# Performance work log

Hardware: AMD Instinct MI355X
Metric: run time of the kernel (lower is better)

## Reference

```python
import math
import jax, jax.numpy as jnp
import numpy as np

HID, HEADS, HEAD_DIM, MLP = 768, 12, 64, 3072
ROT_AXIS = HEAD_DIM // 4  # 16 rotary dims per spatial axis, 48 total
MAX_FREQ = 256.0
EPS_GN, EPS_LN = 1e-6, 1e-5


def setup_inputs() -> dict:
    key = jax.random.key(0)
    ks = jax.random.split(key, 5)
    B, H, W, D = 2, 12, 12, 12
    s = 0.02
    return {
        "x": jax.random.normal(ks[0], (B, HID, H, W, D), jnp.float32),
        "norm1_w": jnp.ones((HID,), jnp.float32),
        "w_fused": jax.random.normal(ks[1], (MLP + 3 * HID, HID), jnp.float32) * s,
        "b_fused": jnp.zeros((MLP + 3 * HID,), jnp.float32),
        "q_gamma": jnp.ones((HEAD_DIM,), jnp.float32),
        "q_beta": jnp.zeros((HEAD_DIM,), jnp.float32),
        "k_gamma": jnp.ones((HEAD_DIM,), jnp.float32),
        "k_beta": jnp.zeros((HEAD_DIM,), jnp.float32),
        "w_attn": jax.random.normal(ks[2], (HID, HID), jnp.float32) * s,
        "w_ff": jax.random.normal(ks[3], (HID, MLP // 2), jnp.float32) * s,
        "b_ff": jnp.zeros((HID,), jnp.float32),
    }


def _layernorm(t, gamma, beta):
    mu = jnp.mean(t, axis=-1, keepdims=True)
    var = jnp.mean((t - mu) ** 2, axis=-1, keepdims=True)
    return (t - mu) / jnp.sqrt(var + EPS_LN) * gamma + beta


def _rotate_half(t):
    # interleaved pairs: (x1, x2) -> (-x2, x1)
    t2 = t.reshape(t.shape[:-1] + (t.shape[-1] // 2, 2))
    return jnp.stack((-t2[..., 1], t2[..., 0]), axis=-1).reshape(t.shape)


def _axial_freqs(H, W, D):
    base = jnp.linspace(1.0, MAX_FREQ / 2, ROT_AXIS // 2) * math.pi  # (8,)
    def ax(n):
        pos = jnp.linspace(-1.0, 1.0, n)
        f = pos[:, None] * base[None, :]          # (n, 8)
        return jnp.repeat(f, 2, axis=-1)          # (n, 16)
    fH = jnp.broadcast_to(ax(H)[:, None, None, :], (H, W, D, ROT_AXIS))
    fW = jnp.broadcast_to(ax(W)[None, :, None, :], (H, W, D, ROT_AXIS))
    fD = jnp.broadcast_to(ax(D)[None, None, :, :], (H, W, D, ROT_AXIS))
    return jnp.concatenate((fH, fW, fD), axis=-1)  # (H, W, D, 48)


def _apply_rope(t, cosf, sinf, rot_dim):
    t_mid, t_right = t[..., :rot_dim], t[..., rot_dim:]
    t_mid = t_mid * cosf + _rotate_half(t_mid) * sinf
    return jnp.concatenate((t_mid, t_right), axis=-1)


def reference(x, norm1_w, w_fused, b_fused, q_gamma, q_beta, k_gamma, k_beta,
              w_attn, w_ff, b_ff):
    B, C, H, W, D = x.shape
    residual = x
    # RMSGroupNorm: norm axes are the spatial dims only (per-channel RMS)
    rms = jnp.sqrt(jnp.mean(x ** 2, axis=(2, 3, 4), keepdims=True) + EPS_GN)
    xn = x / rms * norm1_w[None, :, None, None, None]
    xn = jnp.transpose(xn, (0, 2, 3, 4, 1))  # b h w d c
    fused = jnp.einsum('bhwdc,oc->bhwdo', xn, w_fused) + b_fused
    ff = fused[..., :MLP]
    q = fused[..., MLP:MLP + HID]
    k = fused[..., MLP + HID:MLP + 2 * HID]
    v = fused[..., MLP + 2 * HID:]
    def to_heads(t):  # b h w d (he c) -> b he h w d c
        return jnp.transpose(t.reshape(B, H, W, D, HEADS, HEAD_DIM), (0, 4, 1, 2, 3, 5))
    q, k, v = to_heads(q), to_heads(k), to_heads(v)
    q = _layernorm(q, q_gamma, q_beta)
    k = _layernorm(k, k_gamma, k_beta)
    freqs = _axial_freqs(H, W, D)                 # (H, W, D, 48)
    cosf, sinf = jnp.cos(freqs), jnp.sin(freqs)
    rot_dim = freqs.shape[-1]
    q = _apply_rope(q, cosf, sinf, rot_dim)
    k = _apply_rope(k, cosf, sinf, rot_dim)
    S = H * W * D
    q = q.reshape(B, HEADS, S, HEAD_DIM)
    k = k.reshape(B, HEADS, S, HEAD_DIM)
    v = v.reshape(B, HEADS, S, HEAD_DIM)
    scale = 1.0 / math.sqrt(HEAD_DIM)
    attn = jax.nn.softmax(jnp.einsum('bhsc,bhtc->bhst', q, k) * scale, axis=-1)
    att = jnp.einsum('bhst,bhtc->bhsc', attn, v)
    att = jnp.transpose(att, (0, 2, 1, 3)).reshape(B, H, W, D, HID)
    attn_out = jnp.einsum('bhwdc,oc->bhwdo', att, w_attn)
    ff_x, gate = jnp.split(ff, 2, axis=-1)
    ff_act = jax.nn.silu(gate) * ff_x
    ff_out = jnp.einsum('bhwdc,oc->bhwdo', ff_act, w_ff) + b_ff
    out = attn_out + ff_out
    out = jnp.transpose(out, (0, 4, 1, 2, 3)) + residual
    return out
```

## Files before the change

kernel.cpp:

```cpp
#include <hip/hip_runtime.h>

using bf16 = __bf16;
typedef __attribute__((ext_vector_type(8))) __bf16 bf16x8;
typedef __attribute__((ext_vector_type(4))) float f32x4;

#define HID    768
#define S_TOT  1728
#define MLP_   3072
#define NFUSED 5376
#define HEADS  12
#define HDIM   64
#define ROT    48
#define KCAT   2304

__device__ __forceinline__ void gload16(const void* g, void* l) {
  __builtin_amdgcn_global_load_lds((__attribute__((address_space(1))) void*)g,
                                   (__attribute__((address_space(3))) void*)l,
                                   16, 0, 0);
}

__device__ __forceinline__ float fexp2(float x) {
  float r; asm("v_exp_f32 %0, %1" : "=v"(r) : "v"(x)); return r;
}

__device__ __forceinline__ float wsum64(float v) {
  #pragma unroll
  for (int d = 32; d; d >>= 1) v += __shfl_xor(v, d);
  return v;
}

__global__ __launch_bounds__(256) void k_conv(const float* __restrict__ wf,
    const float* __restrict__ wa, const float* __restrict__ wff,
    bf16* __restrict__ owf, bf16* __restrict__ wcat) {
  int i = blockIdx.x * 256 + threadIdx.x;
  const int nf = NFUSED * HID, na = HID * HID, nff = HID * (MLP_ / 2);
  if (i < nf)  owf[i] = (bf16)wf[i];
  if (i < na)  wcat[(i / HID) * KCAT + (i % HID)] = (bf16)wa[i];
  if (i < nff) wcat[(i / (MLP_ / 2)) * KCAT + HID + (i % (MLP_ / 2))] = (bf16)wff[i];
}

__global__ __launch_bounds__(256) void k_rms(const float* __restrict__ x,
    const float* __restrict__ w, float* __restrict__ scale) {
  int bc = blockIdx.x;
  const float* xp = x + (size_t)bc * S_TOT;
  float s = 0.f;
  for (int i = threadIdx.x; i < S_TOT; i += 256) { float v = xp[i]; s += v * v; }
  s = wsum64(s);
  __shared__ float red[4];
  int lane = threadIdx.x & 63, wv = threadIdx.x >> 6;
  if (lane == 0) red[wv] = s;
  __syncthreads();
  if (threadIdx.x == 0) {
    float t = red[0] + red[1] + red[2] + red[3];
    scale[bc] = w[bc % HID] * rsqrtf(t * (1.f / S_TOT) + 1e-6f);
  }
}

__global__ __launch_bounds__(256) void k_xpose(const float* __restrict__ x,
    const float* __restrict__ scale, bf16* __restrict__ xn) {
  __shared__ float t[32][33];
  int b = blockIdx.z, st = blockIdx.x * 32, ct = blockIdx.y * 32;
  int tx = threadIdx.x & 31, ty = threadIdx.x >> 5;
  #pragma unroll
  for (int i = 0; i < 4; ++i) {
    int c = ct + ty + i * 8;
    t[ty + i * 8][tx] = x[((size_t)b * HID + c) * S_TOT + st + tx] * scale[b * HID + c];
  }
  __syncthreads();
  #pragma unroll
  for (int i = 0; i < 4; ++i) {
    int s = st + ty + i * 8;
    xn[((size_t)b * S_TOT + s) * HID + ct + tx] = (bf16)t[tx][ty + i * 8];
  }
}

__global__ __launch_bounds__(256) void k_rope(float* __restrict__ ct, float* __restrict__ st) {
  int i = blockIdx.x * 256 + threadIdx.x;
  if (i >= S_TOT * ROT) return;
  int s = i / ROT, j = i % ROT;
  int axis = j >> 4, pr = (j & 15) >> 1;
  float base = 3.14159265358979323846f * (1.f + pr * (127.f / 7.f));
  int coord = axis == 0 ? (s / 144) : axis == 1 ? ((s / 12) % 12) : (s % 12);
  float pos = -1.f + coord * (2.f / 11.f);
  float f = pos * base;
  ct[i] = cosf(f); st[i] = sinf(f);
}

template <int BN, int NMAJOR, int MINB>
__global__ __launch_bounds__(256, MINB) void k_gemm(const bf16* __restrict__ A,
    const bf16* __restrict__ Bw, const float* __restrict__ bias,
    void* __restrict__ OutV, int M, int N, int K) {
  extern __shared__ __align__(16) char smem[];
  bf16* aL = (bf16*)smem;
  bf16* bL = (bf16*)(smem + 2 * 8192);
  constexpr int NT = BN / 32;
  constexpr int LPS = 2 + BN / 64;
  const int nT = K / 32;
  int nwg = gridDim.x;
  int cq = nwg >> 3, crr = nwg & 7;
  int xcd = blockIdx.x & 7, pos = blockIdx.x >> 3;
  int idx = (xcd < crr ? xcd * (cq + 1) : crr * (cq + 1) + (xcd - crr) * cq) + pos;
  int ntn = N / BN, nmt = M / 128;
  int m0, n0;
  if (NMAJOR) { n0 = (idx / nmt) * BN; m0 = (idx % nmt) * 128; }
  else        { m0 = (idx / ntn) * 128; n0 = (idx % ntn) * BN; }
  int lane = threadIdx.x & 63, wv = threadIdx.x >> 6;
  int wm = (wv >> 1) * 64, wn = (wv & 1) * (BN / 2);
  int arow = lane >> 2;
  int acs = ((lane & 3) ^ ((lane >> 3) & 3)) * 8;
  int r16 = lane & 15, g8 = (lane >> 4) * 8;
  int swz = ((r16 >> 1) & 3) << 3;
  const bf16* Ag = A + (size_t)m0 * K;
  const bf16* Bg = Bw + (size_t)n0 * K;
  auto stage = [&](int p, int t) {
    int kk = t * 32;
    #pragma unroll
    for (int i = 0; i < 2; ++i) {
      int rb = wv * 32 + i * 16;
      gload16(Ag + (size_t)(rb + arow) * K + kk + acs, aL + p * 4096 + rb * 32);
    }
    #pragma unroll
    for (int i = 0; i < BN / 64; ++i) {
      int rb = wv * (BN / 4) + i * 16;
      gload16(Bg + (size_t)(rb + arow) * K + kk + acs, bL + p * (BN * 32) + rb * 32);
    }
  };
  f32x4 acc[4][NT] = {};
  int p = 0;
  stage(0, 0);
  for (int t = 0; t < nT; ++t) {
    if (t + 1 < nT) {
      stage(p ^ 1, t + 1);
      if constexpr (LPS == 5) asm volatile("s_waitcnt vmcnt(5)\ns_barrier" ::: "memory");
      else if constexpr (LPS == 4) asm volatile("s_waitcnt vmcnt(4)\ns_barrier" ::: "memory");
      else                     asm volatile("s_waitcnt vmcnt(3)\ns_barrier" ::: "memory");
    } else {
      asm volatile("s_waitcnt vmcnt(0)\ns_barrier" ::: "memory");
    }
    bf16x8 af[4], bfr[NT];
    #pragma unroll
    for (int mi = 0; mi < 4; ++mi)
      af[mi] = *(const bf16x8*)(aL + p * 4096 + (wm + mi * 16 + r16) * 32 + (g8 ^ swz));
    #pragma unroll
    for (int ni = 0; ni < NT; ++ni)
      bfr[ni] = *(const bf16x8*)(bL + p * (BN * 32) + (wn + ni * 16 + r16) * 32 + (g8 ^ swz));
    __builtin_amdgcn_s_setprio(1);
    #pragma unroll
    for (int mi = 0; mi < 4; ++mi)
      #pragma unroll
      for (int ni = 0; ni < NT; ++ni)
        acc[mi][ni] = __builtin_amdgcn_mfma_f32_16x16x32_bf16(af[mi], bfr[ni], acc[mi][ni], 0, 0, 0);
    __builtin_amdgcn_s_setprio(0);
    asm volatile("s_barrier" ::: "memory");
    p ^= 1;
  }
  int cr = (lane >> 4) * 4;
  #pragma unroll
  for (int mi = 0; mi < 4; ++mi)
    #pragma unroll
    for (int ni = 0; ni < NT; ++ni) {
      int col = n0 + wn + ni * 16 + r16;
      float bv = bias[col];
      #pragma unroll
      for (int j = 0; j < 4; ++j) {
        int row = m0 + wm + mi * 16 + cr + j;
        ((bf16*)OutV)[(size_t)row * N + col] = (bf16)(acc[mi][ni][j] + bv);
      }
    }
}

__global__ __launch_bounds__(256, 3) void k_gemmO(const bf16* __restrict__ A,
    const bf16* __restrict__ Bw, const float* __restrict__ bias,
    float* __restrict__ Out, const float* __restrict__ X, int M, int N, int K) {
  extern __shared__ __align__(16) char smem[];
  bf16* aL = (bf16*)smem;
  bf16* bL = (bf16*)(smem + 2 * 16384);
  const int nT = K / 64;
  int nwg = gridDim.x;
  int cq = nwg >> 3, crr = nwg & 7;
  int xcd = blockIdx.x & 7, pos = blockIdx.x >> 3;
  int idx = (xcd < crr ? xcd * (cq + 1) : crr * (cq + 1) + (xcd - crr) * cq) + pos;
  int ntn = N / 64;
  int m0 = (idx / ntn) * 128, n0 = (idx % ntn) * 64;
  int lane = threadIdx.x & 63, wv = threadIdx.x >> 6;
  int wm = (wv >> 1) * 64, wn = (wv & 1) * 32;
  int rg = lane >> 3, ch = lane & 7;
  int scs = (ch ^ rg) * 8;
  int r16 = lane & 15, g8 = (lane >> 4) * 8;
  const bf16* Ag = A + (size_t)m0 * K;
  const bf16* Bg = Bw + (size_t)n0 * K;
  auto stage = [&](int p, int t) {
    int kk = t * 64;
    #pragma unroll
    for (int i = 0; i < 4; ++i) {
      int rb = wv * 32 + i * 8;
      gload16(Ag + (size_t)(rb + rg) * K + kk + scs, aL + p * 8192 + rb * 64);
    }
    #pragma unroll
    for (int i = 0; i < 2; ++i) {
      int rb = wv * 16 + i * 8;
      gload16(Bg + (size_t)(rb + rg) * K + kk + scs, bL + p * 4096 + rb * 64);
    }
  };
  f32x4 acc[4][2] = {};
  int p = 0;
  stage(0, 0);
  for (int t = 0; t < nT; ++t) {
    if (t + 1 < nT) {
      stage(p ^ 1, t + 1);
      asm volatile("s_waitcnt vmcnt(6)\ns_barrier" ::: "memory");
    } else {
      asm volatile("s_waitcnt vmcnt(0)\ns_barrier" ::: "memory");
    }
    bf16x8 af[4][2], bfr[2][2];
    #pragma unroll
    for (int kc = 0; kc < 2; ++kc) {
      int ce = ((kc * 4 + (lane >> 4)) ^ (r16 & 7)) * 8;
      #pragma unroll
      for (int mi = 0; mi < 4; ++mi)
        af[mi][kc] = *(const bf16x8*)(aL + p * 8192 + (wm + mi * 16 + r16) * 64 + ce);
      #pragma unroll
      for (int ni = 0; ni < 2; ++ni)
        bfr[ni][kc] = *(const bf16x8*)(bL + p * 4096 + (wn + ni * 16 + r16) * 64 + ce);
    }
    __builtin_amdgcn_s_setprio(1);
    #pragma unroll
    for (int kc = 0; kc < 2; ++kc)
      #pragma unroll
      for (int mi = 0; mi < 4; ++mi)
        #pragma unroll
        for (int ni = 0; ni < 2; ++ni)
          acc[mi][ni] = __builtin_amdgcn_mfma_f32_16x16x32_bf16(af[mi][kc], bfr[ni][kc], acc[mi][ni], 0, 0, 0);
    __builtin_amdgcn_s_setprio(0);
    asm volatile("s_barrier" ::: "memory");
    p ^= 1;
  }
  int cr = (lane >> 4) * 4;
  float* tb = (float*)smem;
  __syncthreads();
  #pragma unroll
  for (int mi = 0; mi < 4; ++mi)
    #pragma unroll
    for (int ni = 0; ni < 2; ++ni) {
      int c = wn + ni * 16 + r16;
      float bv = bias[n0 + c];
      #pragma unroll
      for (int j = 0; j < 4; ++j)
        tb[c * 129 + wm + mi * 16 + cr + j] = acc[mi][ni][j] + bv;
    }
  __syncthreads();
  for (int ci = 0; ci < 16; ++ci) {
    int c = wv * 16 + ci;
    #pragma unroll
    for (int si = 0; si < 2; ++si) {
      int r = si * 64 + lane;
      int m = m0 + r;
      int bb = (m >= S_TOT) ? 1 : 0;
      size_t oidx = ((size_t)bb * HID + n0 + c) * S_TOT + (m - bb * S_TOT);
      Out[oidx] = tb[c * 129 + r] + X[oidx];
    }
  }
}

__global__ __launch_bounds__(256) void k_silu(const bf16* __restrict__ fused, bf16* __restrict__ acat) {
  int idx = blockIdx.x * 256 + threadIdx.x;
  if (idx >= 3456 * 192) return;
  int r = idx / 192, jg = idx % 192;
  bf16x8 xv = *(const bf16x8*)(fused + (size_t)r * NFUSED + jg * 8);
  bf16x8 gv = *(const bf16x8*)(fused + (size_t)r * NFUSED + (MLP_ / 2) + jg * 8);
  bf16x8 o;
  #pragma unroll
  for (int j = 0; j < 8; ++j) {
    float g  = (float)gv[j];
    float xf = (float)xv[j];
    o[j] = (bf16)(g / (1.f + __expf(-g)) * xf);
  }
  *(bf16x8*)(acat + (size_t)r * KCAT + HID + jg * 8) = o;
}

__global__ __launch_bounds__(256) void k_qkv(const bf16* __restrict__ fused,
    const float* __restrict__ ct, const float* __restrict__ st,
    const float* __restrict__ qg, const float* __restrict__ qb,
    const float* __restrict__ kg, const float* __restrict__ kb,
    bf16* __restrict__ qr, bf16* __restrict__ kr, bf16* __restrict__ vt) {
  int bs = blockIdx.x;
  int b = bs / S_TOT, s = bs % S_TOT;
  int lane = threadIdx.x & 63, wv = threadIdx.x >> 6;
  int d = lane;
  float c = 0.f, sn = 0.f;
  if (d < ROT) { c = ct[s * ROT + d]; sn = st[s * ROT + d]; }
  for (int it = 0; it < 9; ++it) {
    int rr = wv * 9 + it;
    int t = rr / HEADS, h = rr % HEADS;
    float v = (float)fused[(size_t)bs * NFUSED + MLP_ + t * HID + h * HDIM + d];
    if (t < 2) {
      float s1 = v, s2 = v * v;
      #pragma unroll
      for (int dd = 32; dd; dd >>= 1) { s1 += __shfl_xor(s1, dd); s2 += __shfl_xor(s2, dd); }
      float mu = s1 * (1.f / 64);
      float var = s2 * (1.f / 64) - mu * mu;
      float vn = (v - mu) * rsqrtf(var + 1e-5f);
      vn = (t == 0) ? (vn * qg[d] + qb[d]) : (vn * kg[d] + kb[d]);
      float o = vn;
      if (d < ROT) {
        float p = __shfl_xor(vn, 1);
        float rot = (d & 1) ? p : -p;
        o = vn * c + rot * sn;
      }
      if (t == 0) o *= 0.18033688f;
      bf16* dst = (t == 0) ? qr : kr;
      dst[((size_t)(b * HEADS + h) * S_TOT + s) * HDIM + d] = (bf16)o;
    } else {
      vt[((size_t)(b * HEADS + h) * HDIM + d) * S_TOT + s] = (bf16)v;
    }
  }
}

__global__ __launch_bounds__(256, 4) void k_attn(const bf16* __restrict__ qr,
    const bf16* __restrict__ kr, const bf16* __restrict__ vt, bf16* __restrict__ acat) {
  __shared__ __align__(16) bf16 kld[2][4096];
  __shared__ __align__(16) bf16 vld[2][4096];
  __shared__ __align__(16) bf16 pld[4][1024];
  int rid = (blockIdx.x & 7) * 81 + (blockIdx.x >> 3);
  int bh = rid / 27, qt = rid % 27;
  int lane = threadIdx.x & 63, wv = threadIdx.x >> 6;
  int r16 = lane & 15, g8 = (lane >> 4) * 8;
  int sw = (r16 & 7) << 3;
  int lsw = (lane & 56) | ((lane ^ (lane >> 3)) & 7);
  const bf16* qbase = qr + ((size_t)bh * S_TOT + qt * 64 + wv * 16) * HDIM;
  bf16x8 qf[2];
  qf[0] = *(const bf16x8*)(qbase + r16 * HDIM + g8);
  qf[1] = *(const bf16x8*)(qbase + r16 * HDIM + 32 + g8);
  asm volatile("s_waitcnt vmcnt(0)" ::: "memory");
  const bf16* kg0 = kr + (size_t)bh * S_TOT * HDIM;
  const bf16* vg0 = vt + (size_t)bh * HDIM * S_TOT;
  auto stage = [&](int buf, int kt) {
    #pragma unroll
    for (int i = 0; i < 2; ++i) {
      int q = wv * 2 + i;
      gload16(kg0 + (size_t)kt * 4096 + q * 512 + lsw * 8, &kld[buf][q * 512]);
      gload16(vg0 + (size_t)(q * 8 + (lane >> 3)) * S_TOT + kt * 64 + (lsw & 7) * 8,
              &vld[buf][q * 512]);
    }
  };
  float m_run[4] = {-1e30f, -1e30f, -1e30f, -1e30f};
  float l_part[4] = {0.f, 0.f, 0.f, 0.f};
  f32x4 acc_o[4] = {};
  stage(0, 0);
  int buf = 0;
  for (int kt = 0; kt < 27; ++kt) {
    if (kt < 26) {
      stage(buf ^ 1, kt + 1);
      asm volatile("s_waitcnt vmcnt(4)\n\ts_barrier" ::: "memory");
    } else {
      asm volatile("s_waitcnt vmcnt(0)\n\ts_barrier" ::: "memory");
    }
    f32x4 sa[4];
    __builtin_amdgcn_s_setprio(1);
    #pragma unroll
    for (int nt = 0; nt < 4; ++nt) {
      sa[nt] = f32x4{0.f, 0.f, 0.f, 0.f};
      #pragma unroll
      for (int kc = 0; kc < 2; ++kc) {
        bf16x8 kf = *(const bf16x8*)(&kld[buf][(nt * 16 + r16) * 64 + ((kc * 32 + g8) ^ sw)]);
        sa[nt] = __builtin_amdgcn_mfma_f32_16x16x32_bf16(qf[kc], kf, sa[nt], 0, 0, 0);
      }
    }
    __builtin_amdgcn_s_setprio(0);
    float lmax[4];
    #pragma unroll
    for (int j = 0; j < 4; ++j)
      lmax[j] = fmaxf(fmaxf(sa[0][j], sa[1][j]), fmaxf(sa[2][j], sa[3][j]));
    bool need = (lmax[0] > m_run[0] + 8.f) || (lmax[1] > m_run[1] + 8.f) ||
                (lmax[2] > m_run[2] + 8.f) || (lmax[3] > m_run[3] + 8.f);
    if (__any(need)) {
      float fac[4];
      #pragma unroll
      for (int j = 0; j < 4; ++j) {
        float tm = lmax[j];
        #pragma unroll
        for (int dd = 1; dd < 16; dd <<= 1) tm = fmaxf(tm, __shfl_xor(tm, dd));
        float mnew = fmaxf(m_run[j], tm);
        fac[j] = fexp2(m_run[j] - mnew);
        m_run[j] = mnew;
        l_part[j] *= fac[j];
      }
      #pragma unroll
      for (int nt = 0; nt < 4; ++nt)
        #pragma unroll
        for (int j = 0; j < 4; ++j) acc_o[nt][j] *= fac[j];
    }
    #pragma unroll
    for (int j = 0; j < 4; ++j) {
      float m = m_run[j];
      #pragma unroll
      for (int nt = 0; nt < 4; ++nt) {
        float pv = fexp2(sa[nt][j] - m);
        sa[nt][j] = pv;
        l_part[j] += pv;
      }
    }
    #pragma unroll
    for (int nt = 0; nt < 4; ++nt)
      #pragma unroll
      for (int j = 0; j < 4; ++j) {
        int rr = (lane >> 4) * 4 + j;
        pld[wv][rr * 64 + ((nt * 16 + r16) ^ ((rr & 7) << 3))] = (bf16)sa[nt][j];
      }
    __builtin_amdgcn_s_setprio(1);
    #pragma unroll
    for (int nt = 0; nt < 4; ++nt)
      #pragma unroll
      for (int kc = 0; kc < 2; ++kc) {
        bf16x8 pf = *(const bf16x8*)(&pld[wv][r16 * 64 + ((kc * 32 + g8) ^ sw)]);
        bf16x8 vf = *(const bf16x8*)(&vld[buf][(nt * 16 + r16) * 64 + ((kc * 32 + g8) ^ sw)]);
        acc_o[nt] = __builtin_amdgcn_mfma_f32_16x16x32_bf16(pf, vf, acc_o[nt], 0, 0, 0);
      }
    __builtin_amdgcn_s_setprio(0);
    asm volatile("s_barrier" ::: "memory");
    buf ^= 1;
  }
  int b = bh / HEADS, h = bh % HEADS;
  #pragma unroll
  for (int j = 0; j < 4; ++j) {
    float l = l_part[j];
    #pragma unroll
    for (int dd = 1; dd < 16; dd <<= 1) l += __shfl_xor(l, dd);
    float inv = 1.f / l;
    int s = qt * 64 + wv * 16 + (lane >> 4) * 4 + j;
    #pragma unroll
    for (int nt = 0; nt < 4; ++nt)
      acat[((size_t)b * S_TOT + s) * KCAT + h * HDIM + nt * 16 + r16] = (bf16)(acc_o[nt][j] * inv);
  }
}

extern "C" void kernel_launch(void* const* d_in, const int* in_sizes, int n_in,
                              void* d_out, int out_size, void* d_ws, size_t ws_size,
                              hipStream_t stream) {
  const float* x   = (const float*)d_in[0];
  const float* n1w = (const float*)d_in[1];
  const float* wf  = (const float*)d_in[2];
  const float* bfu = (const float*)d_in[3];
  const float* qg  = (const float*)d_in[4];
  const float* qb  = (const float*)d_in[5];
  const float* kg  = (const float*)d_in[6];
  const float* kb  = (const float*)d_in[7];
  const float* wa  = (const float*)d_in[8];
  const float* wff = (const float*)d_in[9];
  const float* bff = (const float*)d_in[10];
  float* out = (float*)d_out;

  char* ws = (char*)d_ws;
  size_t off = 0;
  auto alloc = [&](size_t bytes) {
    void* p = ws + off;
    off = (off + bytes + 255) & ~(size_t)255;
    return p;
  };
  const int M = 2 * S_TOT;
  bf16*  wf_b   = (bf16*)alloc((size_t)NFUSED * HID * 2);
  bf16*  wcat   = (bf16*)alloc((size_t)HID * KCAT * 2);
  float* scale  = (float*)alloc(2 * HID * 4);
  bf16*  xn     = (bf16*)alloc((size_t)M * HID * 2);
  float* ctab   = (float*)alloc((size_t)S_TOT * ROT * 4);
  float* stab   = (float*)alloc((size_t)S_TOT * ROT * 4);
  bf16*  fused  = (bf16*)alloc((size_t)M * NFUSED * 2);
  bf16*  qrb    = (bf16*)alloc((size_t)24 * S_TOT * HDIM * 2);
  bf16*  krb    = (bf16*)alloc((size_t)24 * S_TOT * HDIM * 2);
  bf16*  vtb    = (bf16*)alloc((size_t)24 * HDIM * S_TOT * 2);
  bf16*  acat   = (bf16*)alloc((size_t)M * KCAT * 2);
  if (off > ws_size) return;

  const int LDS_QKV = 2 * 8192 + 2 * 192 * 32 * 2;
  const int LDS_MRG = 2 * 16384 + 2 * 4096 * 2;
  hipFuncSetAttribute((const void*)k_gemm<192, 1, 3>, hipFuncAttributeMaxDynamicSharedMemorySize, LDS_QKV);
  hipFuncSetAttribute((const void*)k_gemmO, hipFuncAttributeMaxDynamicSharedMemorySize, LDS_MRG);

  k_conv<<<(NFUSED * HID + 255) / 256, 256, 0, stream>>>(wf, wa, wff, wf_b, wcat);
  k_rms<<<2 * HID, 256, 0, stream>>>(x, n1w, scale);
  k_xpose<<<dim3(S_TOT / 32, HID / 32, 2), 256, 0, stream>>>(x, scale, xn);
  k_rope<<<(S_TOT * ROT + 255) / 256, 256, 0, stream>>>(ctab, stab);
  k_gemm<192, 1, 3><<<(M / 128) * (NFUSED / 192), 256, LDS_QKV, stream>>>(
      xn, wf_b, bfu, fused, M, NFUSED, HID);
  k_silu<<<(M * (MLP_ / 2) / 8 + 255) / 256, 256, 0, stream>>>(fused, acat);
  k_qkv<<<M, 256, 0, stream>>>(fused, ctab, stab, qg, qb, kg, kb, qrb, krb, vtb);
  k_attn<<<648, 256, 0, stream>>>(qrb, krb, vtb, acat);
  k_gemmO<<<(M / 128) * (HID / 64), 256, LDS_MRG, stream>>>(
      acat, wcat, bff, out, x, M, HID, KCAT);
}
```

Measured before the change: 159.4 us.

## Fuse SiLU gating into fused-projection GEMM epilogue via interleaved weight permutation

Permutes the rows of the fused weight and bias so each 32-column group holds 16 ff_x columns next to their 16 gate columns. The GEMM epilogue can then compute silu(gate)*x in registers and write straight into acat. This removes the separate k_silu kernel and avoids writing and re-reading the 3072-wide MLP half of the fused activation buffer. The QKV part now goes to a narrower buffer, which adds permutation work in the conversion kernel and a strided scatter store in the epilogue.

```diff
diff --git a/kernel.cpp b/kernel.cpp
--- a/kernel.cpp
+++ b/kernel.cpp
@@ -12,6 +12,7 @@
 #define HDIM   64
 #define ROT    48
 #define KCAT   2304
+#define NQKV   2304
 
 __device__ __forceinline__ void gload16(const void* g, void* l) {
   __builtin_amdgcn_global_load_lds((__attribute__((address_space(1))) void*)g,
@@ -31,10 +32,20 @@
 
 __global__ __launch_bounds__(256) void k_conv(const float* __restrict__ wf,
     const float* __restrict__ wa, const float* __restrict__ wff,
-    bf16* __restrict__ owf, bf16* __restrict__ wcat) {
+    const float* __restrict__ bfu,
+    bf16* __restrict__ owf, bf16* __restrict__ wcat, float* __restrict__ bperm) {
   int i = blockIdx.x * 256 + threadIdx.x;
   const int nf = NFUSED * HID, na = HID * HID, nff = HID * (MLP_ / 2);
-  if (i < nf)  owf[i] = (bf16)wf[i];
+  auto perm = [](int o) {
+    if (o < 1536) return (o >> 4) * 32 + (o & 15);
+    if (o < 3072) { int g = o - 1536; return (g >> 4) * 32 + 16 + (g & 15); }
+    return o;
+  };
+  if (i < nf) {
+    int o = i / HID, c = i % HID;
+    owf[(size_t)perm(o) * HID + c] = (bf16)wf[i];
+  }
+  if (i < NFUSED) bperm[perm(i)] = bfu[i];
   if (i < na)  wcat[(i / HID) * KCAT + (i % HID)] = (bf16)wa[i];
   if (i < nff) wcat[(i / (MLP_ / 2)) * KCAT + HID + (i % (MLP_ / 2))] = (bf16)wff[i];
 }
@@ -86,24 +97,20 @@
   ct[i] = cosf(f); st[i] = sinf(f);
 }
 
-template <int BN, int NMAJOR, int MINB>
-__global__ __launch_bounds__(256, MINB) void k_gemm(const bf16* __restrict__ A,
+__global__ __launch_bounds__(256, 3) void k_gemmF(const bf16* __restrict__ A,
     const bf16* __restrict__ Bw, const float* __restrict__ bias,
-    void* __restrict__ OutV, int M, int N, int K) {
+    bf16* __restrict__ acat, bf16* __restrict__ qkvb, int M, int N, int K) {
   extern __shared__ __align__(16) char smem[];
   bf16* aL = (bf16*)smem;
   bf16* bL = (bf16*)(smem + 2 * 8192);
-  constexpr int NT = BN / 32;
-  constexpr int LPS = 2 + BN / 64;
+  constexpr int BN = 192, NT = 6;
   const int nT = K / 32;
   int nwg = gridDim.x;
   int cq = nwg >> 3, crr = nwg & 7;
   int xcd = blockIdx.x & 7, pos = blockIdx.x >> 3;
   int idx = (xcd < crr ? xcd * (cq + 1) : crr * (cq + 1) + (xcd - crr) * cq) + pos;
-  int ntn = N / BN, nmt = M / 128;
-  int m0, n0;
-  if (NMAJOR) { n0 = (idx / nmt) * BN; m0 = (idx % nmt) * 128; }
-  else        { m0 = (idx / ntn) * 128; n0 = (idx % ntn) * BN; }
+  int nmt = M / 128;
+  int n0 = (idx / nmt) * BN, m0 = (idx % nmt) * 128;
   int lane = threadIdx.x & 63, wv = threadIdx.x >> 6;
   int wm = (wv >> 1) * 64, wn = (wv & 1) * (BN / 2);
   int arow = lane >> 2;
@@ -120,8 +127,8 @@
       gload16(Ag + (size_t)(rb + arow) * K + kk + acs, aL + p * 4096 + rb * 32);
     }
     #pragma unroll
-    for (int i = 0; i < BN / 64; ++i) {
-      int rb = wv * (BN / 4) + i * 16;
+    for (int i = 0; i < 3; ++i) {
+      int rb = wv * 48 + i * 16;
       gload16(Bg + (size_t)(rb + arow) * K + kk + acs, bL + p * (BN * 32) + rb * 32);
     }
   };
@@ -131,9 +138,7 @@
   for (int t = 0; t < nT; ++t) {
     if (t + 1 < nT) {
       stage(p ^ 1, t + 1);
-      if constexpr (LPS == 5) asm volatile("s_waitcnt vmcnt(5)\ns_barrier" ::: "memory");
-      else if constexpr (LPS == 4) asm volatile("s_waitcnt vmcnt(4)\ns_barrier" ::: "memory");
-      else                     asm volatile("s_waitcnt vmcnt(3)\ns_barrier" ::: "memory");
+      asm volatile("s_waitcnt vmcnt(5)\ns_barrier" ::: "memory");
     } else {
       asm volatile("s_waitcnt vmcnt(0)\ns_barrier" ::: "memory");
     }
@@ -155,18 +160,37 @@
     p ^= 1;
   }
   int cr = (lane >> 4) * 4;
-  #pragma unroll
-  for (int mi = 0; mi < 4; ++mi)
-    #pragma unroll
-    for (int ni = 0; ni < NT; ++ni) {
-      int col = n0 + wn + ni * 16 + r16;
-      float bv = bias[col];
-      #pragma unroll
-      for (int j = 0; j < 4; ++j) {
-        int row = m0 + wm + mi * 16 + cr + j;
-        ((bf16*)OutV)[(size_t)row * N + col] = (bf16)(acc[mi][ni][j] + bv);
-      }
-    }
+  if (n0 < MLP_) {
+    #pragma unroll
+    for (int pp = 0; pp < 3; ++pp) {
+      int base = n0 + wn + pp * 32;
+      int ch = (base >> 5) * 16 + r16;
+      float bx = bias[base + r16], bg = bias[base + 16 + r16];
+      #pragma unroll
+      for (int mi = 0; mi < 4; ++mi)
+        #pragma unroll
+        for (int j = 0; j < 4; ++j) {
+          int row = m0 + wm + mi * 16 + cr + j;
+          float xv = acc[mi][2 * pp][j] + bx;
+          float gv = acc[mi][2 * pp + 1][j] + bg;
+          float sg = gv / (1.f + fexp2(gv * -1.442695041f));
+          acat[(size_t)row * KCAT + HID + ch] = (bf16)(sg * xv);
+        }
+    }
+  } else {
+    #pragma unroll
+    for (int mi = 0; mi < 4; ++mi)
+      #pragma unroll
+      for (int ni = 0; ni < NT; ++ni) {
+        int col = n0 + wn + ni * 16 + r16;
+        float bv = bias[col];
+        #pragma unroll
+        for (int j = 0; j < 4; ++j) {
+          int row = m0 + wm + mi * 16 + cr + j;
+          qkvb[(size_t)row * NQKV + (col - MLP_)] = (bf16)(acc[mi][ni][j] + bv);
+        }
+      }
+  }
 }
 
 __global__ __launch_bounds__(256, 3) void k_gemmO(const bf16* __restrict__ A,
@@ -262,23 +286,7 @@
   }
 }
 
-__global__ __launch_bounds__(256) void k_silu(const bf16* __restrict__ fused, bf16* __restrict__ acat) {
-  int idx = blockIdx.x * 256 + threadIdx.x;
-  if (idx >= 3456 * 192) return;
-  int r = idx / 192, jg = idx % 192;
-  bf16x8 xv = *(const bf16x8*)(fused + (size_t)r * NFUSED + jg * 8);
-  bf16x8 gv = *(const bf16x8*)(fused + (size_t)r * NFUSED + (MLP_ / 2) + jg * 8);
-  bf16x8 o;
-  #pragma unroll
-  for (int j = 0; j < 8; ++j) {
-    float g  = (float)gv[j];
-    float xf = (float)xv[j];
-    o[j] = (bf16)(g / (1.f + __expf(-g)) * xf);
-  }
-  *(bf16x8*)(acat + (size_t)r * KCAT + HID + jg * 8) = o;
-}
-
-__global__ __launch_bounds__(256) void k_qkv(const bf16* __restrict__ fused,
+__global__ __launch_bounds__(256) void k_qkv(const bf16* __restrict__ qkvb,
     const float* __restrict__ ct, const float* __restrict__ st,
     const float* __restrict__ qg, const float* __restrict__ qb,
     const float* __restrict__ kg, const float* __restrict__ kb,
@@ -292,7 +300,7 @@
   for (int it = 0; it < 9; ++it) {
     int rr = wv * 9 + it;
     int t = rr / HEADS, h = rr % HEADS;
-    float v = (float)fused[(size_t)bs * NFUSED + MLP_ + t * HID + h * HDIM + d];
+    float v = (float)qkvb[(size_t)bs * NQKV + t * HID + h * HDIM + d];
     if (t < 2) {
       float s1 = v, s2 = v * v;
       #pragma unroll
@@ -460,11 +468,12 @@
   const int M = 2 * S_TOT;
   bf16*  wf_b   = (bf16*)alloc((size_t)NFUSED * HID * 2);
   bf16*  wcat   = (bf16*)alloc((size_t)HID * KCAT * 2);
+  float* bperm  = (float*)alloc((size_t)NFUSED * 4);
   float* scale  = (float*)alloc(2 * HID * 4);
   bf16*  xn     = (bf16*)alloc((size_t)M * HID * 2);
   float* ctab   = (float*)alloc((size_t)S_TOT * ROT * 4);
   float* stab   = (float*)alloc((size_t)S_TOT * ROT * 4);
-  bf16*  fused  = (bf16*)alloc((size_t)M * NFUSED * 2);
+  bf16*  qkvb   = (bf16*)alloc((size_t)M * NQKV * 2);
   bf16*  qrb    = (bf16*)alloc((size_t)24 * S_TOT * HDIM * 2);
   bf16*  krb    = (bf16*)alloc((size_t)24 * S_TOT * HDIM * 2);
   bf16*  vtb    = (bf16*)alloc((size_t)24 * HDIM * S_TOT * 2);
@@ -473,17 +482,16 @@
 
   const int LDS_QKV = 2 * 8192 + 2 * 192 * 32 * 2;
   const int LDS_MRG = 2 * 16384 + 2 * 4096 * 2;
-  hipFuncSetAttribute((const void*)k_gemm<192, 1, 3>, hipFuncAttributeMaxDynamicSharedMemorySize, LDS_QKV);
+  hipFuncSetAttribute((const void*)k_gemmF, hipFuncAttributeMaxDynamicSharedMemorySize, LDS_QKV);
   hipFuncSetAttribute((const void*)k_gemmO, hipFuncAttributeMaxDynamicSharedMemorySize, LDS_MRG);
 
-  k_conv<<<(NFUSED * HID + 255) / 256, 256, 0, stream>>>(wf, wa, wff, wf_b, wcat);
+  k_conv<<<(NFUSED * HID + 255) / 256, 256, 0, stream>>>(wf, wa, wff, bfu, wf_b, wcat, bperm);
   k_rms<<<2 * HID, 256, 0, stream>>>(x, n1w, scale);
   k_xpose<<<dim3(S_TOT / 32, HID / 32, 2), 256, 0, stream>>>(x, scale, xn);
   k_rope<<<(S_TOT * ROT + 255) / 256, 256, 0, stream>>>(ctab, stab);
-  k_gemm<192, 1, 3><<<(M / 128) * (NFUSED / 192), 256, LDS_QKV, stream>>>(
-      xn, wf_b, bfu, fused, M, NFUSED, HID);
-  k_silu<<<(M * (MLP_ / 2) / 8 + 255) / 256, 256, 0, stream>>>(fused, acat);
-  k_qkv<<<M, 256, 0, stream>>>(fused, ctab, stab, qg, qb, kg, kb, qrb, krb, vtb);
+  k_gemmF<<<(M / 128) * (NFUSED / 192), 256, LDS_QKV, stream>>>(
+      xn, wf_b, bperm, acat, qkvb, M, NFUSED, HID);
+  k_qkv<<<M, 256, 0, stream>>>(qkvb, ctab, stab, qg, qb, kg, kb, qrb, krb, vtb);
   k_attn<<<648, 256, 0, stream>>>(qrb, krb, vtb, acat);
   k_gemmO<<<(M / 128) * (HID / 64), 256, LDS_MRG, stream>>>(
       acat, wcat, bff, out, x, M, HID, KCAT);
```

Result: faster. 154.3 us (-3.2%).
